# Kernel optimization log

Measured on AMD Instinct MI355X. Metric: run time of the kernel, lower is better.

## Reference

```python
import jax, jax.numpy as jnp
import numpy as np

N_NODES = 50000
N_EDGES = 1600000
D_IN = 512
D_OUT = 512


def setup_inputs() -> dict:
    key = jax.random.key(0)
    k1, k2, k3, k4, k5, k6 = jax.random.split(key, 6)
    stdv = 1.0 / np.sqrt(D_OUT)
    x = jax.random.normal(k1, (N_NODES, D_IN), dtype=jnp.float32)
    weight = jax.random.uniform(k2, (D_IN, D_OUT), dtype=jnp.float32, minval=-stdv, maxval=stdv)
    bias = jax.random.uniform(k3, (1, D_OUT), dtype=jnp.float32, minval=-stdv, maxval=stdv)
    edge_val = jax.random.uniform(k4, (N_EDGES,), dtype=jnp.float32)
    edge_row = jax.random.randint(k5, (N_EDGES,), 0, N_NODES, dtype=jnp.int64)
    edge_col = jax.random.randint(k6, (N_EDGES,), 0, N_NODES, dtype=jnp.int64)
    return {"x": x, "weight": weight, "bias": bias,
            "edge_val": edge_val, "edge_row": edge_row, "edge_col": edge_col}


def reference(x, weight, bias, edge_val, edge_row, edge_col):
    # hidden = X @ W  : [N, D_OUT] dense GEMM
    hidden = jnp.matmul(x, weight)
    # spmm: out[i] = sum over edges (i <- j) of adj_val * hidden[j]
    msgs = edge_val[:, None] * hidden[edge_col]            # [E, D_OUT]
    out = jax.ops.segment_sum(msgs, edge_row, num_segments=N_NODES)
    return out + bias
```

## Files before the change

kernel.cpp:

```cpp
#include <hip/hip_runtime.h>

typedef short short8 __attribute__((ext_vector_type(8)));
typedef float v4f   __attribute__((ext_vector_type(4)));

#define N_NODES 50000
#define N_EDGES 1600000
#define DIM     512

__device__ __forceinline__ float bf2f(unsigned short u) {
    unsigned int x = ((unsigned int)u) << 16;
    return __uint_as_float(x);
}
__device__ __forceinline__ unsigned short f2bf(float f) {
    unsigned int x = __float_as_uint(f);
    unsigned int r = x + 0x7fffu + ((x >> 16) & 1u);
    return (unsigned short)(r >> 16);
}

__global__ void detect_kernel(const unsigned int* __restrict__ xw,
                              const int* __restrict__ erow,
                              int* __restrict__ flags) {
    __shared__ int cbf, cz;
    if (threadIdx.x == 0) { cbf = 0; cz = 0; }
    __syncthreads();
    int lb = 0, lz = 0;
    for (int i = threadIdx.x; i < 1024; i += 256) {
        unsigned int w = xw[i];
        unsigned int e0 = (w >> 7) & 0xFFu;
        unsigned int e1 = (w >> 23) & 0xFFu;
        if (e0 >= 0x70u && e0 <= 0x8Fu && e1 >= 0x70u && e1 <= 0x8Fu) lb++;
        if (erow[2 * i + 1] == 0) lz++;
    }
    atomicAdd(&cbf, lb);
    atomicAdd(&cz, lz);
    __syncthreads();
    if (threadIdx.x == 0) {
        flags[0] = (cbf > 512) ? 1 : 0;
        flags[1] = (cz > 512) ? 1 : 0;
    }
}

__global__ void transpose_w(const void* __restrict__ Wv,
                            unsigned short* __restrict__ Wt,
                            const int* __restrict__ flags) {
    __shared__ unsigned short tile[32][33];
    const bool fb = flags[0] != 0;
    int bx = blockIdx.x * 32, by = blockIdx.y * 32;
    int tx = threadIdx.x, ty = threadIdx.y;
    if (fb) {
        const unsigned short* W = (const unsigned short*)Wv;
        for (int r = ty; r < 32; r += 8)
            tile[r][tx] = W[(by + r) * DIM + bx + tx];
    } else {
        const float* W = (const float*)Wv;
        for (int r = ty; r < 32; r += 8)
            tile[r][tx] = f2bf(W[(by + r) * DIM + bx + tx]);
    }
    __syncthreads();
    for (int r = ty; r < 32; r += 8)
        Wt[(bx + r) * DIM + by + tx] = tile[tx][r];
}

#define TM 128
#define TN 128
#define BK 32
#define LP 40

__global__ __launch_bounds__(256) void gemm_kernel(
        const void* __restrict__ Xv,
        const unsigned short* __restrict__ Wt,
        unsigned short* __restrict__ H,
        const int* __restrict__ flags) {
    __shared__ unsigned short lA[TM * LP];
    __shared__ unsigned short lB[TN * LP];

    const bool fb = flags[0] != 0;
    const unsigned short* Xb = (const unsigned short*)Xv;
    const float*          Xf = (const float*)Xv;

    const int t = threadIdx.x;
    const int mBase = blockIdx.y * TM;
    const int nBase = blockIdx.x * TN;
    const int w = t >> 6, lane = t & 63;
    const int lr = lane & 15, quad = lane >> 4;
    const int wr = w >> 1, wc = w & 1;

    v4f acc[4][4];
    #pragma unroll
    for (int i = 0; i < 4; ++i)
        #pragma unroll
        for (int j = 0; j < 4; ++j) acc[i][j] = (v4f)0.0f;

    for (int k0 = 0; k0 < DIM; k0 += BK) {
        #pragma unroll
        for (int rep = 0; rep < 2; ++rep) {
            int idx = rep * 256 + t;
            int r = idx >> 2;
            int cc = (idx & 3) * 8;
            int grow = mBase + r; if (grow >= N_NODES) grow = N_NODES - 1;
            size_t goff = (size_t)grow * DIM + k0 + cc;
            if (fb) {
                uint4 av = *(const uint4*)(Xb + goff);
                *(uint4*)(&lA[r * LP + cc]) = av;
            } else {
                float4 a0 = *(const float4*)(Xf + goff);
                float4 a1 = *(const float4*)(Xf + goff + 4);
                uint4 av;
                av.x = (unsigned int)f2bf(a0.x) | ((unsigned int)f2bf(a0.y) << 16);
                av.y = (unsigned int)f2bf(a0.z) | ((unsigned int)f2bf(a0.w) << 16);
                av.z = (unsigned int)f2bf(a1.x) | ((unsigned int)f2bf(a1.y) << 16);
                av.w = (unsigned int)f2bf(a1.z) | ((unsigned int)f2bf(a1.w) << 16);
                *(uint4*)(&lA[r * LP + cc]) = av;
            }
            uint4 bv = *(const uint4*)(Wt + (size_t)(nBase + r) * DIM + k0 + cc);
            *(uint4*)(&lB[r * LP + cc]) = bv;
        }
        __syncthreads();

        short8 bfr[4];
        #pragma unroll
        for (int j = 0; j < 4; ++j)
            bfr[j] = *(const short8*)(&lB[(wc * 64 + j * 16 + lr) * LP + quad * 8]);
        #pragma unroll
        for (int i = 0; i < 4; ++i) {
            short8 a = *(const short8*)(&lA[(wr * 64 + i * 16 + lr) * LP + quad * 8]);
            #pragma unroll
            for (int j = 0; j < 4; ++j)
                acc[i][j] = __builtin_amdgcn_mfma_f32_16x16x32_bf16(a, bfr[j], acc[i][j], 0, 0, 0);
        }
        __syncthreads();
    }

    #pragma unroll
    for (int i = 0; i < 4; ++i) {
        #pragma unroll
        for (int j = 0; j < 4; ++j) {
            #pragma unroll
            for (int r = 0; r < 4; ++r) {
                int gm = mBase + wr * 64 + i * 16 + quad * 4 + r;
                int gn = nBase + wc * 64 + j * 16 + lr;
                if (gm < N_NODES)
                    H[(size_t)gm * DIM + gn] = f2bf(acc[i][j][r]);
            }
        }
    }
}

__global__ void hist_kernel(const int* __restrict__ row, int* __restrict__ cnt,
                            const int* __restrict__ flags) {
    const bool f64 = flags[1] != 0;
    int i = blockIdx.x * 256 + threadIdx.x;
    if (i < N_EDGES) {
        int r = f64 ? row[2 * (size_t)i] : row[i];
        atomicAdd(&cnt[r], 1);
    }
}

__global__ __launch_bounds__(1024) void scan_kernel(
        const int* __restrict__ cnt, int* __restrict__ start, int* __restrict__ cursor) {
    __shared__ int part[1024];
    const int t = threadIdx.x;
    const int CH = 49;
    int lo = t * CH, hi = lo + CH;
    if (lo > N_NODES) lo = N_NODES;
    if (hi > N_NODES) hi = N_NODES;
    int s = 0;
    for (int i = lo; i < hi; ++i) s += cnt[i];
    part[t] = s;
    __syncthreads();
    for (int off = 1; off < 1024; off <<= 1) {
        int v = (t >= off) ? part[t - off] : 0;
        __syncthreads();
        part[t] += v;
        __syncthreads();
    }
    int run = (t > 0) ? part[t - 1] : 0;
    for (int i = lo; i < hi; ++i) {
        start[i] = run;
        cursor[i] = run;
        run += cnt[i];
    }
    if (t == 0) start[N_NODES] = N_EDGES;
}

__global__ void scatter_kernel(const int* __restrict__ row, const int* __restrict__ col,
                               const void* __restrict__ valv,
                               int* __restrict__ cursor,
                               int* __restrict__ sCol, float* __restrict__ sVal,
                               const int* __restrict__ flags) {
    const bool fb  = flags[0] != 0;
    const bool f64 = flags[1] != 0;
    int i = blockIdx.x * 256 + threadIdx.x;
    if (i < N_EDGES) {
        int r = f64 ? row[2 * (size_t)i] : row[i];
        int c = f64 ? col[2 * (size_t)i] : col[i];
        float v = fb ? bf2f(((const unsigned short*)valv)[i])
                     : ((const float*)valv)[i];
        int p = atomicAdd(&cursor[r], 1);
        sCol[p] = c;
        sVal[p] = v;
    }
}

__global__ __launch_bounds__(256) void gather_kernel(
        const int* __restrict__ start, const int* __restrict__ sCol,
        const float* __restrict__ sVal, const unsigned short* __restrict__ H,
        const void* __restrict__ biasv, void* __restrict__ outv,
        const int* __restrict__ flags) {
    __shared__ int   lc[256];
    __shared__ float lv[256];
    const bool fb = flags[0] != 0;
    const int node = blockIdx.x;
    const int t = threadIdx.x;
    const int s = start[node], e = start[node + 1];
    float a0 = 0.f, a1 = 0.f;
    for (int base = s; base < e; base += 256) {
        int n = e - base; if (n > 256) n = 256;
        if (t < n) { lc[t] = sCol[base + t]; lv[t] = sVal[base + t]; }
        __syncthreads();
        for (int j = 0; j < n; ++j) {
            int c = lc[j];
            float v = lv[j];
            unsigned int h = *(const unsigned int*)(H + (size_t)c * DIM + t * 2);
            a0 += v * bf2f((unsigned short)(h & 0xffffu));
            a1 += v * bf2f((unsigned short)(h >> 16));
        }
        __syncthreads();
    }
    if (fb) {
        unsigned int bb = ((const unsigned int*)biasv)[t];
        a0 += bf2f((unsigned short)(bb & 0xffffu));
        a1 += bf2f((unsigned short)(bb >> 16));
        unsigned int o = (unsigned int)f2bf(a0) | ((unsigned int)f2bf(a1) << 16);
        ((unsigned int*)outv)[(size_t)node * (DIM / 2) + t] = o;
    } else {
        const float* bf = (const float*)biasv;
        a0 += bf[t * 2];
        a1 += bf[t * 2 + 1];
        float2 o; o.x = a0; o.y = a1;
        *(float2*)((float*)outv + (size_t)node * DIM + t * 2) = o;
    }
}

extern "C" void kernel_launch(void* const* d_in, const int* in_sizes, int n_in,
                              void* d_out, int out_size, void* d_ws, size_t ws_size,
                              hipStream_t stream) {
    const void* X    = d_in[0];
    const void* W    = d_in[1];
    const void* bias = d_in[2];
    const void* eval = d_in[3];
    const int*  erow = (const int*)d_in[4];
    const int*  ecol = (const int*)d_in[5];

    char* w = (char*)d_ws;
    size_t o = 0;
    int* flags = (int*)(w + o); o += 16;
    unsigned short* hidden = (unsigned short*)(w + o); o += (size_t)N_NODES * DIM * 2;
    int*   sCol   = (int*)(w + o);   o += (size_t)N_EDGES * 4;
    float* sVal   = (float*)(w + o); o += (size_t)N_EDGES * 4;
    int*   cnt    = (int*)(w + o);   o += 200704;
    int*   start  = (int*)(w + o);   o += 200704;
    int*   cursor = (int*)(w + o);   o += 200704;
    unsigned short* Wt = (unsigned short*)(w + o); o += (size_t)DIM * DIM * 2;

    hipMemsetAsync(cnt, 0, N_NODES * sizeof(int), stream);

    detect_kernel<<<1, 256, 0, stream>>>((const unsigned int*)X, erow, flags);
    transpose_w<<<dim3(16, 16), dim3(32, 8), 0, stream>>>(W, Wt, flags);
    gemm_kernel<<<dim3(DIM / TN, (N_NODES + TM - 1) / TM), 256, 0, stream>>>(X, Wt, hidden, flags);
    hist_kernel<<<(N_EDGES + 255) / 256, 256, 0, stream>>>(erow, cnt, flags);
    scan_kernel<<<1, 1024, 0, stream>>>(cnt, start, cursor);
    scatter_kernel<<<(N_EDGES + 255) / 256, 256, 0, stream>>>(erow, ecol, eval, cursor, sCol, sVal, flags);
    gather_kernel<<<N_NODES, 256, 0, stream>>>(start, sCol, sVal, hidden, bias, d_out, flags);
}
```

Measured before the change: 816.8 us.

## Parallelize CSR scan across blocks and pack col/val into int2 for gather

Replaces the single-block 1024-thread serial-chunk scan with a three-kernel multi-block scan (block sums, serial offsets, per-block scan), so the per-thread strided loops over cnt are coalesced. Packs the sorted column index and edge value into one int2 array, so scatter does one 8-byte store and gather one 8-byte load per edge. The gather drops the shared-memory staging and its barriers and has every thread read the packed edge directly with unrolled FMAs. The extra launches add fixed overhead, and the broadcast edge loads now go through cache instead of LDS.

Result: faster. 700.9 us (-14.2%).

```diff
diff --git a/kernel.cpp b/kernel.cpp
--- a/kernel.cpp
+++ b/kernel.cpp
@@ -6,6 +6,7 @@
 #define N_NODES 50000
 #define N_EDGES 1600000
 #define DIM     512
+#define SCAN_NB 49
 
 __device__ __forceinline__ float bf2f(unsigned short u) {
     unsigned int x = ((unsigned int)u) << 16;
@@ -156,37 +157,70 @@
     }
 }
 
-__global__ __launch_bounds__(1024) void scan_kernel(
-        const int* __restrict__ cnt, int* __restrict__ start, int* __restrict__ cursor) {
-    __shared__ int part[1024];
-    const int t = threadIdx.x;
-    const int CH = 49;
-    int lo = t * CH, hi = lo + CH;
-    if (lo > N_NODES) lo = N_NODES;
-    if (hi > N_NODES) hi = N_NODES;
+__global__ __launch_bounds__(256) void scan1_kernel(const int* __restrict__ cnt,
+                                                    int* __restrict__ bsum) {
+    __shared__ int sh[256];
+    const int b = blockIdx.x, t = threadIdx.x;
+    int base = b * 1024 + t * 4;
     int s = 0;
-    for (int i = lo; i < hi; ++i) s += cnt[i];
-    part[t] = s;
-    __syncthreads();
-    for (int off = 1; off < 1024; off <<= 1) {
-        int v = (t >= off) ? part[t - off] : 0;
-        __syncthreads();
-        part[t] += v;
-        __syncthreads();
-    }
-    int run = (t > 0) ? part[t - 1] : 0;
-    for (int i = lo; i < hi; ++i) {
-        start[i] = run;
-        cursor[i] = run;
-        run += cnt[i];
-    }
-    if (t == 0) start[N_NODES] = N_EDGES;
+    #pragma unroll
+    for (int k = 0; k < 4; ++k) {
+        int i = base + k;
+        if (i < N_NODES) s += cnt[i];
+    }
+    sh[t] = s;
+    __syncthreads();
+    for (int off = 128; off > 0; off >>= 1) {
+        if (t < off) sh[t] += sh[t + off];
+        __syncthreads();
+    }
+    if (t == 0) bsum[b] = sh[0];
+}
+
+__global__ void scan2_kernel(const int* __restrict__ bsum, int* __restrict__ boff,
+                             int* __restrict__ start) {
+    if (threadIdx.x == 0) {
+        int run = 0;
+        for (int b = 0; b < SCAN_NB; ++b) { boff[b] = run; run += bsum[b]; }
+        start[N_NODES] = N_EDGES;
+    }
+}
+
+__global__ __launch_bounds__(256) void scan3_kernel(const int* __restrict__ cnt,
+                                                    const int* __restrict__ boff,
+                                                    int* __restrict__ start,
+                                                    int* __restrict__ cursor) {
+    __shared__ int sh[256];
+    const int b = blockIdx.x, t = threadIdx.x;
+    int base = b * 1024 + t * 4;
+    int v[4];
+    #pragma unroll
+    for (int k = 0; k < 4; ++k) {
+        int i = base + k;
+        v[k] = (i < N_NODES) ? cnt[i] : 0;
+    }
+    int tsum = v[0] + v[1] + v[2] + v[3];
+    sh[t] = tsum;
+    __syncthreads();
+    for (int off = 1; off < 256; off <<= 1) {
+        int x = (t >= off) ? sh[t - off] : 0;
+        __syncthreads();
+        sh[t] += x;
+        __syncthreads();
+    }
+    int excl = sh[t] - tsum + boff[b];
+    #pragma unroll
+    for (int k = 0; k < 4; ++k) {
+        int i = base + k;
+        if (i < N_NODES) { start[i] = excl; cursor[i] = excl; }
+        excl += v[k];
+    }
 }
 
 __global__ void scatter_kernel(const int* __restrict__ row, const int* __restrict__ col,
                                const void* __restrict__ valv,
                                int* __restrict__ cursor,
-                               int* __restrict__ sCol, float* __restrict__ sVal,
+                               int2* __restrict__ sCV,
                                const int* __restrict__ flags) {
     const bool fb  = flags[0] != 0;
     const bool f64 = flags[1] != 0;
@@ -197,35 +231,28 @@
         float v = fb ? bf2f(((const unsigned short*)valv)[i])
                      : ((const float*)valv)[i];
         int p = atomicAdd(&cursor[r], 1);
-        sCol[p] = c;
-        sVal[p] = v;
+        int2 cv; cv.x = c; cv.y = __float_as_int(v);
+        sCV[p] = cv;
     }
 }
 
 __global__ __launch_bounds__(256) void gather_kernel(
-        const int* __restrict__ start, const int* __restrict__ sCol,
-        const float* __restrict__ sVal, const unsigned short* __restrict__ H,
+        const int* __restrict__ start, const int2* __restrict__ sCV,
+        const unsigned short* __restrict__ H,
         const void* __restrict__ biasv, void* __restrict__ outv,
         const int* __restrict__ flags) {
-    __shared__ int   lc[256];
-    __shared__ float lv[256];
     const bool fb = flags[0] != 0;
     const int node = blockIdx.x;
     const int t = threadIdx.x;
     const int s = start[node], e = start[node + 1];
     float a0 = 0.f, a1 = 0.f;
-    for (int base = s; base < e; base += 256) {
-        int n = e - base; if (n > 256) n = 256;
-        if (t < n) { lc[t] = sCol[base + t]; lv[t] = sVal[base + t]; }
-        __syncthreads();
-        for (int j = 0; j < n; ++j) {
-            int c = lc[j];
-            float v = lv[j];
-            unsigned int h = *(const unsigned int*)(H + (size_t)c * DIM + t * 2);
-            a0 += v * bf2f((unsigned short)(h & 0xffffu));
-            a1 += v * bf2f((unsigned short)(h >> 16));
-        }
-        __syncthreads();
+    #pragma unroll 4
+    for (int p = s; p < e; ++p) {
+        int2 cv = sCV[p];
+        float v = __int_as_float(cv.y);
+        unsigned int h = *(const unsigned int*)(H + (size_t)cv.x * DIM + t * 2);
+        a0 = fmaf(v, bf2f((unsigned short)(h & 0xffffu)), a0);
+        a1 = fmaf(v, bf2f((unsigned short)(h >> 16)), a1);
     }
     if (fb) {
         unsigned int bb = ((const unsigned int*)biasv)[t];
@@ -254,14 +281,15 @@
 
     char* w = (char*)d_ws;
     size_t o = 0;
-    int* flags = (int*)(w + o); o += 16;
+    int* flags = (int*)(w + o); o += 256;
     unsigned short* hidden = (unsigned short*)(w + o); o += (size_t)N_NODES * DIM * 2;
-    int*   sCol   = (int*)(w + o);   o += (size_t)N_EDGES * 4;
-    float* sVal   = (float*)(w + o); o += (size_t)N_EDGES * 4;
+    int2*  sCV    = (int2*)(w + o);  o += (size_t)N_EDGES * 8;
     int*   cnt    = (int*)(w + o);   o += 200704;
     int*   start  = (int*)(w + o);   o += 200704;
     int*   cursor = (int*)(w + o);   o += 200704;
     unsigned short* Wt = (unsigned short*)(w + o); o += (size_t)DIM * DIM * 2;
+    int*   bsum   = (int*)(w + o);   o += 256;
+    int*   boff   = (int*)(w + o);   o += 256;
 
     hipMemsetAsync(cnt, 0, N_NODES * sizeof(int), stream);
 
@@ -269,7 +297,9 @@
     transpose_w<<<dim3(16, 16), dim3(32, 8), 0, stream>>>(W, Wt, flags);
     gemm_kernel<<<dim3(DIM / TN, (N_NODES + TM - 1) / TM), 256, 0, stream>>>(X, Wt, hidden, flags);
     hist_kernel<<<(N_EDGES + 255) / 256, 256, 0, stream>>>(erow, cnt, flags);
-    scan_kernel<<<1, 1024, 0, stream>>>(cnt, start, cursor);
-    scatter_kernel<<<(N_EDGES + 255) / 256, 256, 0, stream>>>(erow, ecol, eval, cursor, sCol, sVal, flags);
-    gather_kernel<<<N_NODES, 256, 0, stream>>>(start, sCol, sVal, hidden, bias, d_out, flags);
-}
+    scan1_kernel<<<SCAN_NB, 256, 0, stream>>>(cnt, bsum);
+    scan2_kernel<<<1, 64, 0, stream>>>(bsum, boff, start);
+    scan3_kernel<<<SCAN_NB, 256, 0, stream>>>(cnt, boff, start, cursor);
+    scatter_kernel<<<(N_EDGES + 255) / 256, 256, 0, stream>>>(erow, ecol, eval, cursor, sCV, flags);
+    gather_kernel<<<N_NODES, 256, 0, stream>>>(start, sCV, hidden, bias, d_out, flags);
+}
```
